# Performance work log

Measured on AMD Instinct MI355X. Metric: run time of the kernel, lower is better.

The kernel has to match this reference:

```python
import jax, jax.numpy as jnp
import numpy as np

D_MODEL = 1024
N_HEADS = 16
D_K = D_MODEL // N_HEADS
THETA = 10000.0


def _rope(x, token_positions):
    # x: [b, h, s, d_k]; interleaved RoPE (pairs at even/odd positions)
    half = D_K // 2
    inv_freq = 1.0 / (THETA ** (2.0 * jnp.arange(half, dtype=jnp.float32) / D_K))  # [half]
    angles = token_positions.astype(jnp.float32)[:, None] * inv_freq[None, :]      # [s, half]
    sin, cos = jnp.sin(angles), jnp.cos(angles)
    x_even = x[..., 0::2]
    x_odd = x[..., 1::2]
    out_even = cos * x_even - sin * x_odd
    out_odd = sin * x_even + cos * x_odd
    # interleave back: [..., half, 2] -> [..., d_k]
    return jnp.stack((out_even, out_odd), axis=-1).reshape(x.shape)


def setup_inputs() -> dict:
    key = jax.random.key(0)
    kx, kq, kk, kv, ko = jax.random.split(key, 5)
    b, s = 4, 2048
    std = (2.0 / (D_MODEL + D_MODEL)) ** 0.5
    return {
        "x": jax.random.normal(kx, (b, s, D_MODEL), dtype=jnp.float32),
        "Wq": jax.random.normal(kq, (D_MODEL, D_MODEL), dtype=jnp.float32) * std,
        "Wk": jax.random.normal(kk, (D_MODEL, D_MODEL), dtype=jnp.float32) * std,
        "Wv": jax.random.normal(kv, (D_MODEL, D_MODEL), dtype=jnp.float32) * std,
        "Wo": jax.random.normal(ko, (D_MODEL, D_MODEL), dtype=jnp.float32) * std,
        "token_positions": jnp.arange(s, dtype=jnp.int32),
    }


def reference(x, Wq, Wk, Wv, Wo, token_positions):
    b, s, _ = x.shape
    split = lambda t: t.reshape(b, s, N_HEADS, D_K).transpose(0, 2, 1, 3)  # b h s d
    q = split(x @ Wq.T)
    k = split(x @ Wk.T)
    v = split(x @ Wv.T)
    q = _rope(q, token_positions)
    k = _rope(k, token_positions)
    scores = jnp.einsum("bhnd,bhmd->bhnm", q, k) / jnp.sqrt(jnp.float32(D_K))
    causal = jnp.tril(jnp.ones((s, s), dtype=bool))
    scores = jnp.where(causal, scores, -jnp.inf)
    attn = jax.nn.softmax(scores, axis=-1)
    out = jnp.einsum("bhnm,bhmd->bhnd", attn, v)
    out = out.transpose(0, 2, 1, 3).reshape(b, s, D_MODEL)
    return out @ Wo.T
```

## Files before the change

kernel.cpp:

```cpp
#include <hip/hip_runtime.h>
#include <stdint.h>

typedef __attribute__((ext_vector_type(8))) __bf16 bf16x8;
typedef __attribute__((ext_vector_type(4))) float f32x4;
typedef __attribute__((ext_vector_type(16))) float f32x16;
typedef __attribute__((ext_vector_type(8))) unsigned short ushort8;

__device__ __forceinline__ unsigned short f2bf(float f){
  union { float f; unsigned int i; } v; v.f = f;
  unsigned int r = v.i + 0x7fffu + ((v.i >> 16) & 1u);
  return (unsigned short)(r >> 16);
}
__device__ __forceinline__ void gload16(const void* g, void* l){
  __builtin_amdgcn_global_load_lds((__attribute__((address_space(1))) void*)(g),
                                   (__attribute__((address_space(3))) void*)(l),
                                   16, 0, 0);
}
__device__ __forceinline__ unsigned int cvtpk(float lo, float hi){
  unsigned int r;
  asm("v_cvt_pk_bf16_f32 %0, %1, %2" : "=v"(r) : "v"(lo), "v"(hi));
  return r;
}
__device__ __forceinline__ float fexp2(float x){
  float r; asm("v_exp_f32 %0, %1" : "=v"(r) : "v"(x)); return r;
}
__device__ __forceinline__ bf16x8 ldsw(const char* tile, int row, int colb){
  return *(const bf16x8*)(tile + row*128 + (colb ^ ((row & 7) << 4)));
}

#define SEQ   2048
#define DM    1024
#define NH    16
#define DK    64
#define BATCH 4
#define MTOT  (BATCH*SEQ)
#define NX    (MTOT*DM)
#define NW    (DM*DM)

#define QSCALE 0.18033688011112f

__global__ __launch_bounds__(256) void k_tables(const int* __restrict__ pos,
                                                float* __restrict__ tab)
{
  const int idx = blockIdx.x * 256 + threadIdx.x;
  const int s = idx >> 5, i = idx & 31;
  const float inv = __expf(-0.28782313662425575f * (float)i);
  const float a = (float)pos[s] * inv;
  tab[2*idx]   = cosf(a);
  tab[2*idx+1] = sinf(a);
}

__global__ __launch_bounds__(256) void k_convert(
    const float* __restrict__ x,  const float* __restrict__ wq,
    const float* __restrict__ wk, const float* __restrict__ wv,
    const float* __restrict__ wo,
    unsigned short* __restrict__ xb, unsigned short* __restrict__ wb)
{
  const int tid = blockIdx.x * 256 + threadIdx.x;
  const long long e = (long long)tid * 8;
  const float* src; unsigned short* dst;
  if (e < NX) { src = x + e; dst = xb + e; }
  else {
    long long j = e - NX;
    int seg = (int)(j >> 20);
    long long off = j & 1048575;
    src = (seg==0?wq:seg==1?wk:seg==2?wv:wo) + off;
    dst = wb + (size_t)seg*NW + off;
  }
  const float4 a = *(const float4*)src;
  const float4 b = *(const float4*)(src + 4);
  uint4 o;
  o.x = (unsigned int)f2bf(a.x) | ((unsigned int)f2bf(a.y) << 16);
  o.y = (unsigned int)f2bf(a.z) | ((unsigned int)f2bf(a.w) << 16);
  o.z = (unsigned int)f2bf(b.x) | ((unsigned int)f2bf(b.y) << 16);
  o.w = (unsigned int)f2bf(b.z) | ((unsigned int)f2bf(b.w) << 16);
  *(uint4*)dst = o;
}

#define G0_NT 16
#define G0_BSTR 65536

__global__ __launch_bounds__(512) void k_g0(
    const unsigned short* __restrict__ A,
    const unsigned short* __restrict__ Wb,
    unsigned short* __restrict__ D0,
    unsigned short* __restrict__ D1,
    unsigned short* __restrict__ D2,
    const float* __restrict__ tab)
{
  __shared__ __attribute__((aligned(16))) char lds_[131072];
  const int tid  = threadIdx.x;
  const int lane = tid & 63;
  const int w    = tid >> 6;
  const int wm = w >> 2, wn = w & 3;

  const int bid = blockIdx.x;
  const int tq  = bid >> 3;
  const int m0  = ((bid & 7)*4 + (tq & 3)) * 256;
  const int r   = tq >> 2;
  const int n0  = (r & 3) * 256;
  const int z   = r >> 2;

  const unsigned short* W = Wb + (size_t)z * NW;
  unsigned short* Dh = (z == 0) ? D0 : (z == 1) ? D1 : D2;
  const bool vtr = (z == 2);

  f32x4 acc[8][4];
  #pragma unroll
  for (int i = 0; i < 8; ++i)
    #pragma unroll
    for (int j = 0; j < 4; ++j)
      acc[i][j] = (f32x4)0.0f;

  auto stA = [&](int buf, int t, int l){
    const int id = l*512 + tid;
    const int row = id >> 3, c = id & 7;
    gload16(A + (size_t)(m0 + row)*DM + t*64 + ((c ^ (row & 7)) << 3),
            lds_ + buf*G0_BSTR + id*16);
  };
  auto stB = [&](int buf, int t, int l){
    const int id = l*512 + tid;
    const int row = id >> 3, c = id & 7;
    gload16(W + (size_t)(n0 + row)*DM + t*64 + ((c ^ (row & 7)) << 3),
            lds_ + buf*G0_BSTR + 32768 + id*16);
  };
  auto ldA = [&](const char* Ab_, int i, int kk){
    const int row = wm*128 + i*16 + (lane & 15);
    const int c = (kk*4 + (lane >> 4)) ^ (row & 7);
    return *(const bf16x8*)(Ab_ + row*128 + (c << 4));
  };
  auto ldB = [&](const char* Bb_, int j, int kk){
    const int row = wn*64 + j*16 + (lane & 15);
    const int c = (kk*4 + (lane >> 4)) ^ (row & 7);
    return *(const bf16x8*)(Bb_ + row*128 + (c << 4));
  };

#define G0_MFMA16(IA, IB)                                                               \
  _Pragma("unroll")                                                                     \
  for (int j = 0; j < 4; ++j){                                                          \
    acc[IA][j] = __builtin_amdgcn_mfma_f32_16x16x32_bf16(aF[0][0], bF[j][0], acc[IA][j], 0, 0, 0); \
    acc[IA][j] = __builtin_amdgcn_mfma_f32_16x16x32_bf16(aF[0][1], bF[j][1], acc[IA][j], 0, 0, 0); \
    acc[IB][j] = __builtin_amdgcn_mfma_f32_16x16x32_bf16(aF[1][0], bF[j][0], acc[IB][j], 0, 0, 0); \
    acc[IB][j] = __builtin_amdgcn_mfma_f32_16x16x32_bf16(aF[1][1], bF[j][1], acc[IB][j], 0, 0, 0); \
  }

  #pragma unroll
  for (int l = 0; l < 4; ++l) stA(0, 0, l);
  #pragma unroll
  for (int l = 0; l < 4; ++l) stB(0, 0, l);
  asm volatile("s_waitcnt vmcnt(0)" ::: "memory");
  __builtin_amdgcn_s_barrier();

  for (int t = 0; t < G0_NT; ++t){
    const char* Ab_ = lds_ + (t & 1)*G0_BSTR;
    const char* Bb_ = Ab_ + 32768;
    const int nb = (t + 1) & 1;
    const bool st = (t + 1 < G0_NT);
    bf16x8 aF[2][2], bF[4][2];

    aF[0][0] = ldA(Ab_, 0, 0); aF[0][1] = ldA(Ab_, 0, 1);
    aF[1][0] = ldA(Ab_, 1, 0); aF[1][1] = ldA(Ab_, 1, 1);
    #pragma unroll
    for (int j = 0; j < 4; ++j){ bF[j][0] = ldB(Bb_, j, 0); bF[j][1] = ldB(Bb_, j, 1); }
    if (st){ stA(nb, t+1, 0); stA(nb, t+1, 1); stA(nb, t+1, 2); stA(nb, t+1, 3); }
    __builtin_amdgcn_s_barrier();
    asm volatile("s_waitcnt lgkmcnt(0)" ::: "memory");
    __builtin_amdgcn_s_setprio(1);
    G0_MFMA16(0, 1)
    __builtin_amdgcn_s_setprio(0);
    __builtin_amdgcn_s_barrier();

    aF[0][0] = ldA(Ab_, 2, 0); aF[0][1] = ldA(Ab_, 2, 1);
    aF[1][0] = ldA(Ab_, 3, 0); aF[1][1] = ldA(Ab_, 3, 1);
    if (st){ stB(nb, t+1, 0); stB(nb, t+1, 1); stB(nb, t+1, 2); stB(nb, t+1, 3); }
    __builtin_amdgcn_s_barrier();
    asm volatile("s_waitcnt lgkmcnt(0)" ::: "memory");
    __builtin_amdgcn_s_setprio(1);
    G0_MFMA16(2, 3)
    __builtin_amdgcn_s_setprio(0);
    __builtin_amdgcn_s_barrier();

    aF[0][0] = ldA(Ab_, 4, 0); aF[0][1] = ldA(Ab_, 4, 1);
    aF[1][0] = ldA(Ab_, 5, 0); aF[1][1] = ldA(Ab_, 5, 1);
    __builtin_amdgcn_s_barrier();
    asm volatile("s_waitcnt lgkmcnt(0)" ::: "memory");
    __builtin_amdgcn_s_setprio(1);
    G0_MFMA16(4, 5)
    __builtin_amdgcn_s_setprio(0);
    __builtin_amdgcn_s_barrier();

    aF[0][0] = ldA(Ab_, 6, 0); aF[0][1] = ldA(Ab_, 6, 1);
    aF[1][0] = ldA(Ab_, 7, 0); aF[1][1] = ldA(Ab_, 7, 1);
    __builtin_amdgcn_s_barrier();
    asm volatile("s_waitcnt lgkmcnt(0)" ::: "memory");
    __builtin_amdgcn_s_setprio(1);
    G0_MFMA16(6, 7)
    __builtin_amdgcn_s_setprio(0);
    if (st){
      asm volatile("s_waitcnt vmcnt(0)" ::: "memory");
      __builtin_amdgcn_s_barrier();
    }
  }
#undef G0_MFMA16

  __syncthreads();
  float* T = (float*)lds_;
  #pragma unroll
  for (int h = 0; h < 2; ++h){
    if (h) __syncthreads();
    if (wm == h){
      #pragma unroll
      for (int i = 0; i < 8; ++i)
        #pragma unroll
        for (int j = 0; j < 4; ++j){
          const int n = wn*64 + j*16 + (lane & 15);
          #pragma unroll
          for (int rr = 0; rr < 4; ++rr){
            const int ml = i*16 + ((lane >> 4) << 2) + rr;
            T[ml*256 + (n ^ ((ml & 7) << 2))] = acc[i][j][rr];
          }
        }
    }
    __syncthreads();
    if (vtr){
      const int nl = tid >> 1, sblk = tid & 1;
      const int d = nl & 63, hh = (n0 >> 6) + (nl >> 6);
      const int bidx = m0 >> 11;
      unsigned short* vrow = Dh + (((size_t)(bidx*NH + hh))*DK + d)*SEQ
                               + (m0 & 2047) + h*128;
      #pragma unroll
      for (int c = 0; c < 8; ++c){
        const int s0 = sblk*8 + c*16;
        float v[8];
        #pragma unroll
        for (int j2 = 0; j2 < 8; ++j2)
          v[j2] = T[(s0 + j2)*256 + (nl ^ (((s0 + j2) & 7) << 2))];
        uint4 ov;
        ov.x = cvtpk(v[0], v[1]); ov.y = cvtpk(v[2], v[3]);
        ov.z = cvtpk(v[4], v[5]); ov.w = cvtpk(v[6], v[7]);
        *(uint4*)(vrow + s0) = ov;
      }
    } else {
      const float scale = (z == 0) ? QSCALE : 1.0f;
      #pragma unroll
      for (int k = 0; k < 8; ++k){
        const int cid  = k*512 + tid;
        const int nb2  = (cid & 31) * 8;
        const int sp_l = cid >> 5;
        const int sw   = (sp_l & 7) << 2;
        const f32x4 c0 = *(const f32x4*)&T[sp_l*256 + (nb2 ^ sw)];
        const f32x4 c1 = *(const f32x4*)&T[sp_l*256 + ((nb2 + 4) ^ sw)];
        const int mg = m0 + h*128 + sp_l;
        const int bidx = mg >> 11, sp = mg & 2047;
        const int d8 = nb2 & 63;
        const float4 t01 = *(const float4*)&tab[(size_t)sp*64 + d8];
        const float4 t23 = *(const float4*)&tab[(size_t)sp*64 + d8 + 4];
        const unsigned int u0 = cvtpk((t01.x*c0[0] - t01.y*c0[1])*scale,
                                      (t01.y*c0[0] + t01.x*c0[1])*scale);
        const unsigned int u1 = cvtpk((t01.z*c0[2] - t01.w*c0[3])*scale,
                                      (t01.w*c0[2] + t01.z*c0[3])*scale);
        const unsigned int u2 = cvtpk((t23.x*c1[0] - t23.y*c1[1])*scale,
                                      (t23.y*c1[0] + t23.x*c1[1])*scale);
        const unsigned int u3 = cvtpk((t23.z*c1[2] - t23.w*c1[3])*scale,
                                      (t23.w*c1[2] + t23.z*c1[3])*scale);
        const int hh = (n0 >> 6) + (nb2 >> 6);
        uint4 ov; ov.x = u0; ov.y = u1; ov.z = u2; ov.w = u3;
        *(uint4*)(Dh + ((size_t)((bidx*NH + hh)*SEQ + sp))*DK + d8) = ov;
      }
    }
  }
}

#define BK64 64
#define NT   (DM/BK64)
#define ABUF 32768
#define BSTRIDE 49152

template<int MODE>
__global__ __launch_bounds__(512, 2) void k_gemm(
    const unsigned short* __restrict__ A,
    const unsigned short* __restrict__ Wb,
    float* __restrict__ Dout)
{
  __shared__ __attribute__((aligned(16))) char lds_[3*BSTRIDE];
  const int tid  = threadIdx.x;
  const int lane = tid & 63;
  const int w    = tid >> 6;
  const int wm = w >> 1, wn = w & 1;

  const int bid = blockIdx.x;
  const int tq  = bid >> 3;
  const int m0  = ((bid & 7)*4 + (tq & 3)) * 256;
  const int n0  = (tq >> 2) * 128;

  const unsigned short* W = Wb;

  f32x4 acc[4][4];
  #pragma unroll
  for (int i = 0; i < 4; ++i)
    #pragma unroll
    for (int j = 0; j < 4; ++j)
      acc[i][j] = (f32x4)0.0f;

  auto stA = [&](int buf, int t, int l){
    const int k0 = t * BK64;
    const int id = l*512 + tid;
    const int row = id >> 3, c = id & 7;
    gload16(A + (size_t)(m0 + row)*DM + k0 + ((c ^ (row & 7)) << 3),
            lds_ + buf*BSTRIDE + id*16);
  };
  auto stB = [&](int buf, int t, int l){
    const int k0 = t * BK64;
    const int id = l*512 + tid;
    const int row = id >> 3, c = id & 7;
    gload16(W + (size_t)(n0 + row)*DM + k0 + ((c ^ (row & 7)) << 3),
            lds_ + buf*BSTRIDE + ABUF + id*16);
  };
  auto ldA = [&](const char* Ab_, int i, int kk){
    const int row = wm*64 + i*16 + (lane & 15);
    const int c = (kk*4 + (lane >> 4)) ^ (row & 7);
    return *(const bf16x8*)(Ab_ + row*128 + (c << 4));
  };
  auto ldB = [&](const char* Bb_, int j, int kk){
    const int row = wn*64 + j*16 + (lane & 15);
    const int c = (kk*4 + (lane >> 4)) ^ (row & 7);
    return *(const bf16x8*)(Bb_ + row*128 + (c << 4));
  };

  #pragma unroll
  for (int l = 0; l < 4; ++l) stA(0, 0, l);
  stB(0, 0, 0); stB(0, 0, 1);
  #pragma unroll
  for (int l = 0; l < 4; ++l) stA(1, 1, l);
  stB(1, 1, 0); stB(1, 1, 1);
  asm volatile("s_waitcnt vmcnt(6)" ::: "memory");
  __builtin_amdgcn_s_barrier();

  int rb = 0, sb = 2;
  for (int t = 0; t < NT; ++t){
    const char* Ab_ = lds_ + rb*BSTRIDE;
    const char* Bb_ = Ab_ + ABUF;
    const bool st = (t + 2 < NT);
    bf16x8 aF0, aF1, bF[4];

    aF0 = ldA(Ab_, 0, 0); aF1 = ldA(Ab_, 1, 0);
    bF[0] = ldB(Bb_, 0, 0); bF[1] = ldB(Bb_, 1, 0);
    bF[2] = ldB(Bb_, 2, 0); bF[3] = ldB(Bb_, 3, 0);
    if (st){ stA(sb, t+2, 0); stA(sb, t+2, 1); }
    __builtin_amdgcn_s_barrier();
    asm volatile("s_waitcnt lgkmcnt(0)" ::: "memory");
    __builtin_amdgcn_s_setprio(1);
    #pragma unroll
    for (int j = 0; j < 4; ++j){
      acc[0][j] = __builtin_amdgcn_mfma_f32_16x16x32_bf16(aF0, bF[j], acc[0][j], 0, 0, 0);
      acc[1][j] = __builtin_amdgcn_mfma_f32_16x16x32_bf16(aF1, bF[j], acc[1][j], 0, 0, 0);
    }
    __builtin_amdgcn_s_setprio(0);
    __builtin_amdgcn_s_barrier();

    aF0 = ldA(Ab_, 2, 0); aF1 = ldA(Ab_, 3, 0);
    if (st){ stA(sb, t+2, 2); stA(sb, t+2, 3); }
    __builtin_amdgcn_s_barrier();
    asm volatile("s_waitcnt lgkmcnt(0)" ::: "memory");
    __builtin_amdgcn_s_setprio(1);
    #pragma unroll
    for (int j = 0; j < 4; ++j){
      acc[2][j] = __builtin_amdgcn_mfma_f32_16x16x32_bf16(aF0, bF[j], acc[2][j], 0, 0, 0);
      acc[3][j] = __builtin_amdgcn_mfma_f32_16x16x32_bf16(aF1, bF[j], acc[3][j], 0, 0, 0);
    }
    __builtin_amdgcn_s_setprio(0);
    __builtin_amdgcn_s_barrier();

    aF0 = ldA(Ab_, 0, 1); aF1 = ldA(Ab_, 1, 1);
    bF[0] = ldB(Bb_, 0, 1); bF[1] = ldB(Bb_, 1, 1);
    bF[2] = ldB(Bb_, 2, 1); bF[3] = ldB(Bb_, 3, 1);
    if (st){ stB(sb, t+2, 0); stB(sb, t+2, 1); }
    __builtin_amdgcn_s_barrier();
    asm volatile("s_waitcnt lgkmcnt(0)" ::: "memory");
    __builtin_amdgcn_s_setprio(1);
    #pragma unroll
    for (int j = 0; j < 4; ++j){
      acc[0][j] = __builtin_amdgcn_mfma_f32_16x16x32_bf16(aF0, bF[j], acc[0][j], 0, 0, 0);
      acc[1][j] = __builtin_amdgcn_mfma_f32_16x16x32_bf16(aF1, bF[j], acc[1][j], 0, 0, 0);
    }
    __builtin_amdgcn_s_setprio(0);
    __builtin_amdgcn_s_barrier();

    aF0 = ldA(Ab_, 2, 1); aF1 = ldA(Ab_, 3, 1);
    __builtin_amdgcn_s_barrier();
    asm volatile("s_waitcnt lgkmcnt(0)" ::: "memory");
    __builtin_amdgcn_s_setprio(1);
    #pragma unroll
    for (int j = 0; j < 4; ++j){
      acc[2][j] = __builtin_amdgcn_mfma_f32_16x16x32_bf16(aF0, bF[j], acc[2][j], 0, 0, 0);
      acc[3][j] = __builtin_amdgcn_mfma_f32_16x16x32_bf16(aF1, bF[j], acc[3][j], 0, 0, 0);
    }
    __builtin_amdgcn_s_setprio(0);
    if (t < NT-2)       asm volatile("s_waitcnt vmcnt(6)" ::: "memory");
    else if (t == NT-2) asm volatile("s_waitcnt vmcnt(0)" ::: "memory");
    if (t < NT-1) __builtin_amdgcn_s_barrier();

    rb = (rb == 2) ? 0 : rb + 1;
    sb = (sb == 2) ? 0 : sb + 1;
  }

  __syncthreads();
  {
    float* T = (float*)lds_;
    #pragma unroll
    for (int i = 0; i < 4; ++i)
      #pragma unroll
      for (int j = 0; j < 4; ++j){
        const int n = wn*64 + j*16 + (lane & 15);
        #pragma unroll
        for (int rr = 0; rr < 4; ++rr){
          const int m = wm*64 + i*16 + ((lane >> 4) << 2) + rr;
          T[m*128 + (n ^ ((m & 7) << 2))] = acc[i][j][rr];
        }
      }
  }
  __syncthreads();
  const float* T = (const float*)lds_;
  #pragma unroll
  for (int k = 0; k < 8; ++k){
    const int cid = k*512 + tid;
    const int d8   = cid & 7;
    const int sp_l = (cid >> 3) & 255;
    const int h    = cid >> 11;
    const int nb   = h*64 + d8*8;
    const int sw   = (sp_l & 7) << 2;
    const f32x4 c0 = *(const f32x4*)&T[sp_l*128 + (nb ^ sw)];
    const f32x4 c1 = *(const f32x4*)&T[sp_l*128 + ((nb + 4) ^ sw)];
    float* dst = Dout + (size_t)(m0 + sp_l)*DM + n0 + nb;
    *(f32x4*)dst = c0;
    *(f32x4*)(dst + 4) = c1;
  }
}

__global__ __launch_bounds__(512, 4) void k_attn(const unsigned short* __restrict__ Qh,
                                                 const unsigned short* __restrict__ Kh,
                                                 const unsigned short* __restrict__ Vt,
                                                 unsigned short* __restrict__ Ab)
{
  __shared__ uint4 ldsu[4096];
  char* base = (char*)ldsu;
  const int tid  = threadIdx.x;
  const int lane = tid & 63;
  const int w    = tid >> 6;
  const int ww   = w & 3;
  const int g    = w >> 2;
  const int tl   = tid & 255;
  const int l31  = lane & 31;
  const int hl   = lane >> 5;
  char* gb = base + g*32768;

  const int jj = blockIdx.x, bh = blockIdx.y;
  const unsigned short* Qb = Qh + (size_t)bh*(SEQ*DK);
  const unsigned short* Kb = Kh + (size_t)bh*(SEQ*DK);
  const unsigned short* Vb = Vt + (size_t)bh*(SEQ*DK);
  const int b = bh >> 4, hd = bh & 15;

  for (int pass = 0; pass < 2; ++pass){
    const int qt = pass ? jj : 15 - jj;
    const int q0 = qt * 128;
    const int qbase = q0 + ww*32;

    bf16x8 qf[4];
    #pragma unroll
    for (int t = 0; t < 4; ++t)
      qf[t] = *(const bf16x8*)(Qb + (size_t)(qbase + l31)*DK + t*16 + hl*8);

    f32x16 acc0 = (f32x16)0.0f, acc1 = (f32x16)0.0f;
    float lsum = 0.0f;

    const int nk = qt + 1;
    const int tbase = g * nk;
    const int wqmax = qbase + 31;

    auto stage = [&](int buf, int ktile){
      const int k0s = ktile * 64;
      char* Kd = gb + buf*16384;
      char* Vd = Kd + 8192;
      #pragma unroll
      for (int cc = 0; cc < 2; ++cc){
        const int f = cc*256 + tl;
        const int r = f >> 3, slot = f & 7;
        const int sw = ((slot ^ (r & 7)) << 3);
        gload16(Kb + (size_t)(k0s + r)*DK + sw, Kd + (cc*256 + ww*64)*16);
        gload16(Vb + (size_t)r*SEQ + k0s + sw, Vd + (cc*256 + ww*64)*16);
      }
    };

    if (pass) __syncthreads();
    stage(0, tbase);
    __syncthreads();
    int cur = 0;

    for (int kt = 0; kt < nk; ++kt){
      const int k0 = (tbase + kt) * 64;
      if (kt + 1 < nk) stage(cur ^ 1, tbase + kt + 1);
      if (k0 <= wqmax){
        const char* Ks = gb + cur*16384;
        const char* Vs = Ks + 8192;

        f32x16 sv0 = (f32x16)0.0f, sv1 = (f32x16)0.0f;
        __builtin_amdgcn_s_setprio(1);
        #pragma unroll
        for (int t = 0; t < 4; ++t){
          const int colb = t*32 + hl*16;
          const bf16x8 a0 = ldsw(Ks, l31, colb);
          const bf16x8 a1 = ldsw(Ks, 32 + l31, colb);
          sv0 = __builtin_amdgcn_mfma_f32_32x32x16_bf16(a0, qf[t], sv0, 0, 0, 0);
          sv1 = __builtin_amdgcn_mfma_f32_32x32x16_bf16(a1, qf[t], sv1, 0, 0, 0);
        }
        __builtin_amdgcn_s_setprio(0);

        if (k0 + 63 > qbase){
          const int q = qbase + l31;
          #pragma unroll
          for (int j = 0; j < 16; ++j){
            const int kv = k0 + (j&3) + 8*(j>>2) + 4*hl;
            if (kv > q)      sv0[j] = -1e30f;
            if (kv + 32 > q) sv1[j] = -1e30f;
          }
        }

        #pragma unroll
        for (int j = 0; j < 16; ++j){
          sv0[j] = fexp2(sv0[j]);
          sv1[j] = fexp2(sv1[j]);
        }
        float ts[8];
        #pragma unroll
        for (int j = 0; j < 8; ++j)
          ts[j] = (sv0[j] + sv0[j+8]) + (sv1[j] + sv1[j+8]);
        #pragma unroll
        for (int off = 4; off; off >>= 1)
          #pragma unroll
          for (int j = 0; j < off; ++j)
            ts[j] += ts[j+off];
        lsum += ts[0] + __shfl_xor(ts[0], 32, 64);

        __builtin_amdgcn_s_setprio(1);
        #pragma unroll
        for (int t = 0; t < 4; ++t){
          f32x16& s = (t < 2) ? sv0 : sv1;
          const int b0v = (t & 1) * 8;
          const unsigned int A0 = cvtpk(s[b0v+0], s[b0v+1]);
          const unsigned int A1 = cvtpk(s[b0v+2], s[b0v+3]);
          const unsigned int B0 = cvtpk(s[b0v+4], s[b0v+5]);
          const unsigned int B1 = cvtpk(s[b0v+6], s[b0v+7]);
          const unsigned int s0 = hl ? A0 : B0;
          const unsigned int s1 = hl ? A1 : B1;
          const unsigned int r0 = (unsigned int)__shfl_xor((int)s0, 32, 64);
          const unsigned int r1 = (unsigned int)__shfl_xor((int)s1, 32, 64);
          union { unsigned int u[4]; bf16x8 v; } f;
          f.u[0] = hl ? r0 : A0; f.u[1] = hl ? r1 : A1;
          f.u[2] = hl ? B0 : r0; f.u[3] = hl ? B1 : r1;
          const int colb = t*32 + hl*16;
          const bf16x8 v0 = ldsw(Vs, l31, colb);
          const bf16x8 v1 = ldsw(Vs, 32 + l31, colb);
          acc0 = __builtin_amdgcn_mfma_f32_32x32x16_bf16(v0, f.v, acc0, 0, 0, 0);
          acc1 = __builtin_amdgcn_mfma_f32_32x32x16_bf16(v1, f.v, acc1, 0, 0, 0);
        }
        __builtin_amdgcn_s_setprio(0);
      }
      __syncthreads();
      cur ^= 1;
    }

    if (g == 1){
      char* cw = base + ww*9216 + lane*144;
      #pragma unroll
      for (int q4 = 0; q4 < 4; ++q4){
        *(f32x4*)(cw + q4*16)      = (f32x4){acc0[4*q4], acc0[4*q4+1], acc0[4*q4+2], acc0[4*q4+3]};
        *(f32x4*)(cw + 64 + q4*16) = (f32x4){acc1[4*q4], acc1[4*q4+1], acc1[4*q4+2], acc1[4*q4+3]};
      }
      *(float*)(cw + 128) = lsum;
    }
    __syncthreads();
    if (g == 0){
      const char* cr = base + ww*9216 + lane*144;
      const float l1 = *(const float*)(cr + 128);
      const float linv = 1.0f / (lsum + l1);
      unsigned short* orow = Ab + ((size_t)(b*SEQ + qbase + l31))*DM + hd*DK;
      #pragma unroll
      for (int mt = 0; mt < 2; ++mt){
        #pragma unroll
        for (int g4 = 0; g4 < 4; ++g4){
          const f32x16& a = mt ? acc1 : acc0;
          const f32x4 o = *(const f32x4*)(cr + mt*64 + g4*16);
          const unsigned int u0 = cvtpk((a[4*g4+0] + o[0])*linv, (a[4*g4+1] + o[1])*linv);
          const unsigned int u1 = cvtpk((a[4*g4+2] + o[2])*linv, (a[4*g4+3] + o[3])*linv);
          *(unsigned long long*)(orow + mt*32 + g4*8 + hl*4) =
              (unsigned long long)u0 | ((unsigned long long)u1 << 32);
        }
      }
    }
  }
}

extern "C" void kernel_launch(void* const* d_in, const int* in_sizes, int n_in,
                              void* d_out, int out_size, void* d_ws, size_t ws_size,
                              hipStream_t stream)
{
  (void)in_sizes; (void)n_in; (void)out_size;
  const float* x  = (const float*)d_in[0];
  const float* wq = (const float*)d_in[1];
  const float* wk = (const float*)d_in[2];
  const float* wv = (const float*)d_in[3];
  const float* wo = (const float*)d_in[4];
  const int* pos  = (const int*)d_in[5];
  float* out = (float*)d_out;

  if (ws_size < 92800000u) return;
  char* ws = (char*)d_ws;
  unsigned short* xb = (unsigned short*)(ws);
  unsigned short* wb = (unsigned short*)(ws + 16777216);
  unsigned short* Qh = (unsigned short*)(ws + 25165824);
  unsigned short* Kh = (unsigned short*)(ws + 41943040);
  unsigned short* Vt = (unsigned short*)(ws + 75497472);
  float* tab         = (float*)(ws + 92274688);

  k_tables  <<<256, 256, 0, stream>>>(pos, tab);
  k_convert <<<6144, 256, 0, stream>>>(x, wq, wk, wv, wo, xb, wb);
  k_g0      <<<384, 512, 0, stream>>>(xb, wb, Qh, Kh, Vt, tab);
  k_attn    <<<dim3(8, 64), 512, 0, stream>>>(Qh, Kh, Vt, xb);
  k_gemm<1> <<<256, 512, 0, stream>>>(xb, wb + 3*NW, out);
}
```

Baseline: 168.3 us.

## Shrink QKV GEMM tile to 128x256 with triple-buffered LDS pipeline

The fused QKV projection kernel now uses 128-row M tiles instead of 256, which doubles the grid to 768 blocks so the machine's CUs are filled better. The LDS pipeline goes from double to triple buffering, prefetching two K-steps ahead with partial vmcnt waits, and warps are laid out 4x2 instead of 2x4. The goal is to fix wave-quantization tail effects and hide global-load latency. In exchange, A/B reuse per block is lower, each block has less MFMA work per barrier, and the epilogue writes back in smaller halves.

```diff
diff --git a/kernel.cpp b/kernel.cpp
--- a/kernel.cpp
+++ b/kernel.cpp
@@ -78,7 +78,7 @@
 }
 
 #define G0_NT 16
-#define G0_BSTR 65536
+#define G0_BSTR 49152
 
 __global__ __launch_bounds__(512) void k_g0(
     const unsigned short* __restrict__ A,
@@ -88,16 +88,16 @@
     unsigned short* __restrict__ D2,
     const float* __restrict__ tab)
 {
-  __shared__ __attribute__((aligned(16))) char lds_[131072];
+  __shared__ __attribute__((aligned(16))) char lds_[3*G0_BSTR];
   const int tid  = threadIdx.x;
   const int lane = tid & 63;
   const int w    = tid >> 6;
-  const int wm = w >> 2, wn = w & 3;
+  const int wm = w >> 1, wn = w & 1;
 
   const int bid = blockIdx.x;
   const int tq  = bid >> 3;
-  const int m0  = ((bid & 7)*4 + (tq & 3)) * 256;
-  const int r   = tq >> 2;
+  const int m0  = ((bid & 7)*8 + (tq & 7)) * 128;
+  const int r   = tq >> 3;
   const int n0  = (r & 3) * 256;
   const int z   = r >> 2;
 
@@ -105,11 +105,11 @@
   unsigned short* Dh = (z == 0) ? D0 : (z == 1) ? D1 : D2;
   const bool vtr = (z == 2);
 
-  f32x4 acc[8][4];
-  #pragma unroll
-  for (int i = 0; i < 8; ++i)
-    #pragma unroll
-    for (int j = 0; j < 4; ++j)
+  f32x4 acc[2][8];
+  #pragma unroll
+  for (int i = 0; i < 2; ++i)
+    #pragma unroll
+    for (int j = 0; j < 8; ++j)
       acc[i][j] = (f32x4)0.0f;
 
   auto stA = [&](int buf, int t, int l){
@@ -122,101 +122,85 @@
     const int id = l*512 + tid;
     const int row = id >> 3, c = id & 7;
     gload16(W + (size_t)(n0 + row)*DM + t*64 + ((c ^ (row & 7)) << 3),
-            lds_ + buf*G0_BSTR + 32768 + id*16);
+            lds_ + buf*G0_BSTR + 16384 + id*16);
   };
   auto ldA = [&](const char* Ab_, int i, int kk){
-    const int row = wm*128 + i*16 + (lane & 15);
+    const int row = wm*32 + i*16 + (lane & 15);
     const int c = (kk*4 + (lane >> 4)) ^ (row & 7);
     return *(const bf16x8*)(Ab_ + row*128 + (c << 4));
   };
   auto ldB = [&](const char* Bb_, int j, int kk){
-    const int row = wn*64 + j*16 + (lane & 15);
+    const int row = wn*128 + j*16 + (lane & 15);
     const int c = (kk*4 + (lane >> 4)) ^ (row & 7);
     return *(const bf16x8*)(Bb_ + row*128 + (c << 4));
   };
 
-#define G0_MFMA16(IA, IB)                                                               \
-  _Pragma("unroll")                                                                     \
-  for (int j = 0; j < 4; ++j){                                                          \
-    acc[IA][j] = __builtin_amdgcn_mfma_f32_16x16x32_bf16(aF[0][0], bF[j][0], acc[IA][j], 0, 0, 0); \
-    acc[IA][j] = __builtin_amdgcn_mfma_f32_16x16x32_bf16(aF[0][1], bF[j][1], acc[IA][j], 0, 0, 0); \
-    acc[IB][j] = __builtin_amdgcn_mfma_f32_16x16x32_bf16(aF[1][0], bF[j][0], acc[IB][j], 0, 0, 0); \
-    acc[IB][j] = __builtin_amdgcn_mfma_f32_16x16x32_bf16(aF[1][1], bF[j][1], acc[IB][j], 0, 0, 0); \
-  }
-
-  #pragma unroll
-  for (int l = 0; l < 4; ++l) stA(0, 0, l);
+  stA(0, 0, 0); stA(0, 0, 1);
   #pragma unroll
   for (int l = 0; l < 4; ++l) stB(0, 0, l);
-  asm volatile("s_waitcnt vmcnt(0)" ::: "memory");
+  stA(1, 1, 0); stA(1, 1, 1);
+  #pragma unroll
+  for (int l = 0; l < 4; ++l) stB(1, 1, l);
+  asm volatile("s_waitcnt vmcnt(6)" ::: "memory");
   __builtin_amdgcn_s_barrier();
 
+  int rb = 0, sb = 2;
   for (int t = 0; t < G0_NT; ++t){
-    const char* Ab_ = lds_ + (t & 1)*G0_BSTR;
-    const char* Bb_ = Ab_ + 32768;
-    const int nb = (t + 1) & 1;
-    const bool st = (t + 1 < G0_NT);
-    bf16x8 aF[2][2], bF[4][2];
-
-    aF[0][0] = ldA(Ab_, 0, 0); aF[0][1] = ldA(Ab_, 0, 1);
-    aF[1][0] = ldA(Ab_, 1, 0); aF[1][1] = ldA(Ab_, 1, 1);
-    #pragma unroll
-    for (int j = 0; j < 4; ++j){ bF[j][0] = ldB(Bb_, j, 0); bF[j][1] = ldB(Bb_, j, 1); }
-    if (st){ stA(nb, t+1, 0); stA(nb, t+1, 1); stA(nb, t+1, 2); stA(nb, t+1, 3); }
+    const char* Ab_ = lds_ + rb*G0_BSTR;
+    const char* Bb_ = Ab_ + 16384;
+    const bool st = (t + 2 < G0_NT);
+    bf16x8 aF0, aF1, bF[8];
+
+    aF0 = ldA(Ab_, 0, 0); aF1 = ldA(Ab_, 1, 0);
+    #pragma unroll
+    for (int j = 0; j < 8; ++j) bF[j] = ldB(Bb_, j, 0);
+    if (st){ stA(sb, t+2, 0); stA(sb, t+2, 1); stB(sb, t+2, 0); }
     __builtin_amdgcn_s_barrier();
     asm volatile("s_waitcnt lgkmcnt(0)" ::: "memory");
     __builtin_amdgcn_s_setprio(1);
-    G0_MFMA16(0, 1)
+    #pragma unroll
+    for (int j = 0; j < 8; ++j){
+      acc[0][j] = __builtin_amdgcn_mfma_f32_16x16x32_bf16(aF0, bF[j], acc[0][j], 0, 0, 0);
+      acc[1][j] = __builtin_amdgcn_mfma_f32_16x16x32_bf16(aF1, bF[j], acc[1][j], 0, 0, 0);
+    }
     __builtin_amdgcn_s_setprio(0);
     __builtin_amdgcn_s_barrier();
 
-    aF[0][0] = ldA(Ab_, 2, 0); aF[0][1] = ldA(Ab_, 2, 1);
-    aF[1][0] = ldA(Ab_, 3, 0); aF[1][1] = ldA(Ab_, 3, 1);
-    if (st){ stB(nb, t+1, 0); stB(nb, t+1, 1); stB(nb, t+1, 2); stB(nb, t+1, 3); }
+    aF0 = ldA(Ab_, 0, 1); aF1 = ldA(Ab_, 1, 1);
+    #pragma unroll
+    for (int j = 0; j < 8; ++j) bF[j] = ldB(Bb_, j, 1);
+    if (st){ stB(sb, t+2, 1); stB(sb, t+2, 2); stB(sb, t+2, 3); }
     __builtin_amdgcn_s_barrier();
     asm volatile("s_waitcnt lgkmcnt(0)" ::: "memory");
     __builtin_amdgcn_s_setprio(1);
-    G0_MFMA16(2, 3)
+    #pragma unroll
+    for (int j = 0; j < 8; ++j){
+      acc[0][j] = __builtin_amdgcn_mfma_f32_16x16x32_bf16(aF0, bF[j], acc[0][j], 0, 0, 0);
+      acc[1][j] = __builtin_amdgcn_mfma_f32_16x16x32_bf16(aF1, bF[j], acc[1][j], 0, 0, 0);
+    }
     __builtin_amdgcn_s_setprio(0);
-    __builtin_amdgcn_s_barrier();
-
-    aF[0][0] = ldA(Ab_, 4, 0); aF[0][1] = ldA(Ab_, 4, 1);
-    aF[1][0] = ldA(Ab_, 5, 0); aF[1][1] = ldA(Ab_, 5, 1);
-    __builtin_amdgcn_s_barrier();
-    asm volatile("s_waitcnt lgkmcnt(0)" ::: "memory");
-    __builtin_amdgcn_s_setprio(1);
-    G0_MFMA16(4, 5)
-    __builtin_amdgcn_s_setprio(0);
-    __builtin_amdgcn_s_barrier();
-
-    aF[0][0] = ldA(Ab_, 6, 0); aF[0][1] = ldA(Ab_, 6, 1);
-    aF[1][0] = ldA(Ab_, 7, 0); aF[1][1] = ldA(Ab_, 7, 1);
-    __builtin_amdgcn_s_barrier();
-    asm volatile("s_waitcnt lgkmcnt(0)" ::: "memory");
-    __builtin_amdgcn_s_setprio(1);
-    G0_MFMA16(6, 7)
-    __builtin_amdgcn_s_setprio(0);
-    if (st){
-      asm volatile("s_waitcnt vmcnt(0)" ::: "memory");
-      __builtin_amdgcn_s_barrier();
-    }
+    if (t < G0_NT-2)       asm volatile("s_waitcnt vmcnt(6)" ::: "memory");
+    else if (t == G0_NT-2) asm volatile("s_waitcnt vmcnt(0)" ::: "memory");
+    if (t < G0_NT-1) __builtin_amdgcn_s_barrier();
+
+    rb = (rb == 2) ? 0 : rb + 1;
+    sb = (sb == 2) ? 0 : sb + 1;
   }
-#undef G0_MFMA16
 
   __syncthreads();
   float* T = (float*)lds_;
   #pragma unroll
   for (int h = 0; h < 2; ++h){
     if (h) __syncthreads();
-    if (wm == h){
+    if ((wm >> 1) == h){
       #pragma unroll
-      for (int i = 0; i < 8; ++i)
-        #pragma unroll
-        for (int j = 0; j < 4; ++j){
-          const int n = wn*64 + j*16 + (lane & 15);
+      for (int i = 0; i < 2; ++i)
+        #pragma unroll
+        for (int j = 0; j < 8; ++j){
+          const int n = wn*128 + j*16 + (lane & 15);
           #pragma unroll
           for (int rr = 0; rr < 4; ++rr){
-            const int ml = i*16 + ((lane >> 4) << 2) + rr;
+            const int ml = (wm & 1)*32 + i*16 + ((lane >> 4) << 2) + rr;
             T[ml*256 + (n ^ ((ml & 7) << 2))] = acc[i][j][rr];
           }
         }
@@ -227,9 +211,9 @@
       const int d = nl & 63, hh = (n0 >> 6) + (nl >> 6);
       const int bidx = m0 >> 11;
       unsigned short* vrow = Dh + (((size_t)(bidx*NH + hh))*DK + d)*SEQ
-                               + (m0 & 2047) + h*128;
+                               + (m0 & 2047) + h*64;
       #pragma unroll
-      for (int c = 0; c < 8; ++c){
+      for (int c = 0; c < 4; ++c){
         const int s0 = sblk*8 + c*16;
         float v[8];
         #pragma unroll
@@ -243,14 +227,14 @@
     } else {
       const float scale = (z == 0) ? QSCALE : 1.0f;
       #pragma unroll
-      for (int k = 0; k < 8; ++k){
+      for (int k = 0; k < 4; ++k){
         const int cid  = k*512 + tid;
         const int nb2  = (cid & 31) * 8;
         const int sp_l = cid >> 5;
         const int sw   = (sp_l & 7) << 2;
         const f32x4 c0 = *(const f32x4*)&T[sp_l*256 + (nb2 ^ sw)];
         const f32x4 c1 = *(const f32x4*)&T[sp_l*256 + ((nb2 + 4) ^ sw)];
-        const int mg = m0 + h*128 + sp_l;
+        const int mg = m0 + h*64 + sp_l;
         const int bidx = mg >> 11, sp = mg & 2047;
         const int d8 = nb2 & 63;
         const float4 t01 = *(const float4*)&tab[(size_t)sp*64 + d8];
@@ -624,7 +608,7 @@
 
   k_tables  <<<256, 256, 0, stream>>>(pos, tab);
   k_convert <<<6144, 256, 0, stream>>>(x, wq, wk, wv, wo, xb, wb);
-  k_g0      <<<384, 512, 0, stream>>>(xb, wb, Qh, Kh, Vt, tab);
+  k_g0      <<<768, 512, 0, stream>>>(xb, wb, Qh, Kh, Vt, tab);
   k_attn    <<<dim3(8, 64), 512, 0, stream>>>(Qh, Kh, Vt, xb);
   k_gemm<1> <<<256, 512, 0, stream>>>(xb, wb + 3*NW, out);
 }
```

Measured after the change: 166.9 us. No clear change (-0.8%).
